# Kernel optimization log

Hardware: AMD Instinct MI355X
Metric: run time of the kernel (lower is better)

The kernel has to match this reference:

```python
import jax, jax.numpy as jnp
import numpy as np

K_DIM = 1024
HEADS = 16


def setup_inputs() -> dict:
    key = jax.random.key(0)
    ks = jax.random.split(key, 8)
    b, t, tc, k = 2, 2048, 2048, K_DIM
    scale = 1.0 / np.sqrt(k)
    x = jax.random.normal(ks[0], (b, t, k), dtype=jnp.float32)
    context = jax.random.normal(ks[1], (b, tc, k), dtype=jnp.float32)
    Wq = jax.random.normal(ks[2], (k, k), dtype=jnp.float32) * scale
    Wk = jax.random.normal(ks[3], (k, k), dtype=jnp.float32) * scale
    Wv = jax.random.normal(ks[4], (k, k), dtype=jnp.float32) * scale
    Wo = jax.random.normal(ks[5], (k, k), dtype=jnp.float32) * scale
    bo = jax.random.normal(ks[6], (k,), dtype=jnp.float32) * 0.01
    return {"x": x, "context": context, "Wq": Wq, "Wk": Wk, "Wv": Wv, "Wo": Wo, "bo": bo}


def reference(x, context, Wq, Wk, Wv, Wo, bo):
    b, t, e = x.shape
    tc = context.shape[1]
    h = HEADS
    s = e // h
    # Linear(k,k,bias=False): y = x @ W.T
    q = (x @ Wq.T).reshape(b, t, h, s)
    k_ = (context @ Wk.T).reshape(b, tc, h, s)
    v = (context @ Wv.T).reshape(b, tc, h, s)
    # scale q and k each by e**-0.25 (net 1/sqrt(e), note: full embed dim, not head dim)
    inv4 = e ** (-0.25)
    q = q * inv4
    k_ = k_ * inv4
    # scores: [b, h, t, tc]
    dot = jnp.einsum('bthd,bchd->bhtc', q, k_)
    attn = jax.nn.softmax(dot, axis=-1)
    out = jnp.einsum('bhtc,bchd->bthd', attn, v).reshape(b, t, e)
    return out @ Wo.T + bo
```

## Files before the change

kernel.cpp:

```cpp
#include <hip/hip_runtime.h>
#include <stdint.h>

typedef unsigned short u16;
typedef unsigned int u32;
typedef __attribute__((ext_vector_type(4))) float f32x4;
typedef __attribute__((ext_vector_type(16))) float f32x16;
typedef __attribute__((ext_vector_type(8))) __bf16 bf16x8;
typedef __attribute__((ext_vector_type(8))) u16 u16x8;

constexpr int NB = 2, NT = 2048, NTC = 2048, NE = 1024, NH = 16, ND = 64;
constexpr int MTOK = NB * NT;
constexpr int KDIM = NE;
constexpr float QK_SCALE = (float)(0.17677669529663687 * 1.2011224087864498);
constexpr float FIXED_M = 24.0f;

__device__ __forceinline__ u16 f2bf(float f) {
  union { float f; uint32_t u; } v; v.f = f;
  uint32_t r = v.u + 0x7FFFu + ((v.u >> 16) & 1u);
  return (u16)(r >> 16);
}

__device__ __forceinline__ float fexp2(float x) {
#if __has_builtin(__builtin_amdgcn_exp2f)
  return __builtin_amdgcn_exp2f(x);
#else
  return exp2f(x);
#endif
}

__device__ __forceinline__ u32 cvtpk(float lo, float hi) {
  u32 r;
  asm("v_cvt_pk_bf16_f32 %0, %1, %2" : "=v"(r) : "v"(lo), "v"(hi));
  return r;
}

__device__ __forceinline__ void plswap(u32& a, u32& b) {
  asm("v_permlane32_swap_b32 %0, %1" : "+v"(a), "+v"(b));
}

__device__ __forceinline__ void gload16(const void* g, void* lds) {
  __builtin_amdgcn_global_load_lds(
      (const __attribute__((address_space(1))) unsigned int*)g,
      (__attribute__((address_space(3))) unsigned int*)lds, 16, 0, 0);
}

__device__ __forceinline__ f32x4 mfma16x16(bf16x8 a, bf16x8 b, f32x4 c) {
  return __builtin_amdgcn_mfma_f32_16x16x32_bf16(a, b, c, 0, 0, 0);
}
__device__ __forceinline__ f32x16 mfma32x32(bf16x8 a, bf16x8 b, f32x16 c) {
  return __builtin_amdgcn_mfma_f32_32x32x16_bf16(a, b, c, 0, 0, 0);
}

__device__ __forceinline__ int swz(int row, int part) {
  return row * 128 + ((part ^ (row & 7)) << 4);
}

__device__ __forceinline__ u16x8 cast8(const float4* p, float scale) {
  float4 a = p[0], b = p[1];
  u16x8 r;
  r[0] = f2bf(a.x * scale); r[1] = f2bf(a.y * scale);
  r[2] = f2bf(a.z * scale); r[3] = f2bf(a.w * scale);
  r[4] = f2bf(b.x * scale); r[5] = f2bf(b.y * scale);
  r[6] = f2bf(b.z * scale); r[7] = f2bf(b.w * scale);
  return r;
}

__global__ void cast_all(const float* __restrict__ x, const float* __restrict__ ctx,
                         const float* __restrict__ Wq, const float* __restrict__ Wk,
                         const float* __restrict__ Wv, const float* __restrict__ Wo,
                         u16* __restrict__ xb, u16* __restrict__ cb,
                         u16* __restrict__ wb) {
  int i = blockIdx.x * blockDim.x + threadIdx.x;
  const float* src; u16* dst; int j; float scale = 1.0f;
  if (i < 524288) { src = x; dst = xb; j = i; }
  else if (i < 1048576) { src = ctx; dst = cb; j = i - 524288; }
  else {
    int k = i - 1048576;
    int which = k >> 17; j = k & 131071;
    src = (which == 0) ? Wq : (which == 1) ? Wk : (which == 2) ? Wv : Wo;
    scale = (which < 2) ? QK_SCALE : 1.0f;
    dst = wb + (size_t)which * (NE * KDIM);
  }
  *((u16x8*)dst + j) = cast8((const float4*)src + (size_t)j * 2, scale);
}

__global__ __launch_bounds__(256)
void gemm_qkv(const u16* __restrict__ xb, const u16* __restrict__ cb,
              const u16* __restrict__ wqb, const u16* __restrict__ wkvb,
              u16* __restrict__ Qb, u16* __restrict__ KVb) {
  __shared__ __align__(16) u16 Al[64 * 64];
  __shared__ __align__(16) u16 Bl[128 * 64];
  const int tid = threadIdx.x, w = tid >> 6, l = tid & 63;
  const int l15 = l & 15, l4 = l >> 4;
  const int wm = w >> 1, wn = w & 1;

  const int bid = blockIdx.x;
  const bool isQ = bid < 512;
  const u16* A; const u16* Bm; int mbase, nbase;
  if (isQ) { A = xb; Bm = wqb; nbase = (bid & 7) * 128; mbase = (bid >> 3) * 64; }
  else { int b2 = bid - 512; A = cb; Bm = wkvb; nbase = (b2 & 15) * 128; mbase = (b2 >> 4) * 64; }

  f32x4 acc[2][4] = {};
  const char* Ab = (const char*)(A + (size_t)mbase * KDIM);
  const char* Bb = (const char*)(Bm + (size_t)nbase * KDIM);

  for (int k0 = 0; k0 < KDIM; k0 += 64) {
#pragma unroll
    for (int s = 0; s < 2; ++s) {
      int i = (w * 2 + s) * 64 + l;
      int row = i >> 3, part = i & 7;
      int gofs = row * (KDIM * 2) + k0 * 2 + ((part ^ (row & 7)) << 4);
      gload16(Ab + gofs, (char*)Al + (w * 2 + s) * 1024);
    }
#pragma unroll
    for (int s = 0; s < 4; ++s) {
      int i = (w * 4 + s) * 64 + l;
      int row = i >> 3, part = i & 7;
      int gofs = row * (KDIM * 2) + k0 * 2 + ((part ^ (row & 7)) << 4);
      gload16(Bb + gofs, (char*)Bl + (w * 4 + s) * 1024);
    }
    __syncthreads();
#pragma unroll
    for (int kc = 0; kc < 2; ++kc) {
      bf16x8 af[2], bfr[4];
#pragma unroll
      for (int mt = 0; mt < 2; ++mt) {
        int r = wm * 32 + mt * 16 + l15;
        af[mt] = *(const bf16x8*)((const char*)Al + swz(r, kc * 4 + l4));
      }
#pragma unroll
      for (int nt = 0; nt < 4; ++nt) {
        int r = wn * 64 + nt * 16 + l15;
        bfr[nt] = *(const bf16x8*)((const char*)Bl + swz(r, kc * 4 + l4));
      }
#pragma unroll
      for (int mt = 0; mt < 2; ++mt)
#pragma unroll
        for (int nt = 0; nt < 4; ++nt)
          acc[mt][nt] = mfma16x16(af[mt], bfr[nt], acc[mt][nt]);
    }
    __syncthreads();
  }

#pragma unroll
  for (int mt = 0; mt < 2; ++mt) {
#pragma unroll
    for (int nt = 0; nt < 4; ++nt) {
      int col = nbase + wn * 64 + nt * 16 + l15;
      int mrow0 = mbase + wm * 32 + mt * 16 + l4 * 4;
#pragma unroll
      for (int r = 0; r < 4; ++r) {
        int m = mrow0 + r;
        float v = acc[mt][nt][r];
        if (isQ) {
          int b = m >> 11, t = m & (NT - 1), h = col >> 6, d = col & (ND - 1);
          Qb[((size_t)(b * NH + h) * NT + t) * ND + d] = f2bf(v);
        } else {
          int b = m >> 11, tc = m & (NTC - 1);
          int h = (col >> 6) & 15, d = col & (ND - 1);
          size_t base = ((size_t)((b * NH + h) * 32 + (tc >> 6))) * 4096;
          if (col < 1024) {
            size_t idx = base + (size_t)(d >> 3) * 512 + (size_t)(tc & 63) * 8 + (d & 7);
            KVb[idx] = f2bf(v);
          } else {
            size_t idx = base + (size_t)((tc & 63) >> 3) * 512 + (size_t)d * 8 + (tc & 7);
            KVb[4194304 + idx] = f2bf(v);
          }
        }
      }
    }
  }
}

__device__ __forceinline__ void gemm_loop(const char* Ab, const char* Bb,
                                          u16* Al, u16* Bl, int tid,
                                          f32x4 (&acc)[2][4]) {
  const int w = tid >> 6, l = tid & 63;
  const int l15 = l & 15, l4 = l >> 4;
  const int wm = w >> 1, wn = w & 1;

  auto stage = [&](int buf, int k0) {
#pragma unroll
    for (int s = 0; s < 2; ++s) {
      int i = (w * 2 + s) * 64 + l;
      int row = i >> 3, part = i & 7;
      int gofs = row * (KDIM * 2) + k0 * 2 + ((part ^ (row & 7)) << 4);
      gload16(Ab + gofs, (char*)(Al + buf * 4096) + (w * 2 + s) * 1024);
    }
#pragma unroll
    for (int s = 0; s < 4; ++s) {
      int i = (w * 4 + s) * 64 + l;
      int row = i >> 3, part = i & 7;
      int gofs = row * (KDIM * 2) + k0 * 2 + ((part ^ (row & 7)) << 4);
      gload16(Bb + gofs, (char*)(Bl + buf * 8192) + (w * 4 + s) * 1024);
    }
  };

  stage(0, 0);
  stage(1, 64);

  for (int it = 0; it < 16; ++it) {
    const int cur = it & 1;
    if (it < 15) asm volatile("s_waitcnt vmcnt(6)" ::: "memory");
    else         asm volatile("s_waitcnt vmcnt(0)" ::: "memory");
    __builtin_amdgcn_s_barrier();
    const char* Ac = (const char*)(Al + cur * 4096);
    const char* Bc = (const char*)(Bl + cur * 8192);
#pragma unroll
    for (int kc = 0; kc < 2; ++kc) {
      bf16x8 af[2], bfr[4];
#pragma unroll
      for (int mt = 0; mt < 2; ++mt)
        af[mt] = *(const bf16x8*)(Ac + swz(wm * 32 + mt * 16 + l15, kc * 4 + l4));
#pragma unroll
      for (int nt = 0; nt < 4; ++nt)
        bfr[nt] = *(const bf16x8*)(Bc + swz(wn * 64 + nt * 16 + l15, kc * 4 + l4));
#pragma unroll
      for (int mt = 0; mt < 2; ++mt)
#pragma unroll
        for (int nt = 0; nt < 4; ++nt)
          acc[mt][nt] = mfma16x16(af[mt], bfr[nt], acc[mt][nt]);
    }
    __builtin_amdgcn_s_barrier();
    if (it < 14) stage(cur, (it + 2) * 64);
  }
}

__global__ __launch_bounds__(256)
void gemm_out(const u16* __restrict__ A, const u16* __restrict__ Bm,
              float* __restrict__ Cout, const float* __restrict__ bias) {
  __shared__ __align__(16) u16 Al[2][64 * 64];
  __shared__ __align__(16) u16 Bl[2][128 * 64];
  const int tid = threadIdx.x, w = tid >> 6, l = tid & 63;
  const int l15 = l & 15, l4 = l >> 4;
  const int wm = w >> 1, wn = w & 1;

  int bid = blockIdx.x;
  bid = (bid & 7) * 64 + (bid >> 3);
  const int mbase = (bid >> 3) * 64, nbase = (bid & 7) * 128;

  f32x4 acc[2][4] = {};
  gemm_loop((const char*)(A + (size_t)mbase * KDIM),
            (const char*)(Bm + (size_t)nbase * KDIM),
            &Al[0][0], &Bl[0][0], tid, acc);

#pragma unroll
  for (int mt = 0; mt < 2; ++mt) {
#pragma unroll
    for (int nt = 0; nt < 4; ++nt) {
      int col = nbase + wn * 64 + nt * 16 + l15;
      int mrow0 = mbase + wm * 32 + mt * 16 + l4 * 4;
#pragma unroll
      for (int r = 0; r < 4; ++r)
        Cout[(size_t)(mrow0 + r) * NE + col] = acc[mt][nt][r] + bias[col];
    }
  }
}

__global__ __launch_bounds__(128, 2)
void attn_fwd(const u16* __restrict__ Q, const u16* __restrict__ K,
              const u16* __restrict__ Vt, u16* __restrict__ O) {
  __shared__ float Ol[64 * 64];
  __shared__ float Ll[64];
  const int tid = threadIdx.x, wid = tid >> 6, l = tid & 63;
  const int l31 = l & 31, hi = l >> 5;

  int n = blockIdx.x;
  int work = (n & 7) * 128 + (n >> 3);
  const int bh = work >> 5, qx = work & 31;
  const int b = bh >> 4, h = bh & 15;
  const int qbase = qx * 64;

  const char* Kb = (const char*)(K + (size_t)bh * 32 * 4096);
  const char* Vb = (const char*)(Vt + (size_t)bh * 32 * 4096);
  const u16* Qb = Q + (size_t)bh * NT * ND;

  auto kaddr = [&](int t32, int kc) {
    return Kb + (size_t)(t32 >> 1) * 8192 + (size_t)(kc * 2 + hi) * 1024
              + (size_t)((t32 & 1) * 32 + l31) * 16;
  };
  auto vaddr = [&](int t32, int j) {
    return Vb + (size_t)(t32 >> 1) * 8192
              + (size_t)((t32 & 1) * 4 + (j >> 1) * 2 + hi) * 1024
              + (size_t)((j & 1) * 32 + l31) * 16;
  };

  bf16x8 qf[2][4];
#pragma unroll
  for (int qt = 0; qt < 2; ++qt)
#pragma unroll
    for (int kc = 0; kc < 4; ++kc)
      qf[qt][kc] = *(const bf16x8*)(Qb + (size_t)(qbase + qt * 32 + l31) * ND + kc * 16 + hi * 8);

  f32x16 oacc[2][2] = {};
  f32x16 lacc[2] = {};
  f32x16 minit;
#pragma unroll
  for (int r = 0; r < 16; ++r) minit[r] = -FIXED_M;

  const int tbase = wid * 32;

  bf16x8 kfA[4], kfB[4], vf[4];
#pragma unroll
  for (int kc = 0; kc < 4; ++kc) kfA[kc] = *(const bf16x8*)kaddr(tbase, kc);

  for (int it2 = 0; it2 < 16; ++it2) {
    const int tA = tbase + it2 * 2, tB = tA + 1;

#pragma unroll
    for (int j = 0; j < 4; ++j) vf[j] = *(const bf16x8*)vaddr(tA, j);
#pragma unroll
    for (int kc = 0; kc < 4; ++kc) kfB[kc] = *(const bf16x8*)kaddr(tB, kc);
#pragma unroll
    for (int qt = 0; qt < 2; ++qt) {
      f32x16 sv = minit;
#pragma unroll
      for (int kc = 0; kc < 4; ++kc) sv = mfma32x32(kfA[kc], qf[qt][kc], sv);
#pragma unroll
      for (int r = 0; r < 16; ++r) { sv[r] = fexp2(sv[r]); lacc[qt][r] += sv[r]; }
      bf16x8 pa0, pa1;
      {
        u32 a1 = cvtpk(sv[0], sv[1]), b1 = cvtpk(sv[4], sv[5]);
        u32 a2 = cvtpk(sv[2], sv[3]), b2 = cvtpk(sv[6], sv[7]);
        plswap(a1, b1); plswap(a2, b2);
        u32 a3 = cvtpk(sv[8], sv[9]), b3 = cvtpk(sv[12], sv[13]);
        u32 a4 = cvtpk(sv[10], sv[11]), b4 = cvtpk(sv[14], sv[15]);
        plswap(a3, b3); plswap(a4, b4);
        union { u32 u[4]; bf16x8 v; } ua, ub;
        ua.u[0] = a1; ua.u[1] = a2; ua.u[2] = b1; ua.u[3] = b2;
        ub.u[0] = a3; ub.u[1] = a4; ub.u[2] = b3; ub.u[3] = b4;
        pa0 = ua.v; pa1 = ub.v;
      }
      oacc[qt][0] = mfma32x32(pa0, vf[0], oacc[qt][0]);
      oacc[qt][1] = mfma32x32(pa0, vf[1], oacc[qt][1]);
      oacc[qt][0] = mfma32x32(pa1, vf[2], oacc[qt][0]);
      oacc[qt][1] = mfma32x32(pa1, vf[3], oacc[qt][1]);
    }

#pragma unroll
    for (int j = 0; j < 4; ++j) vf[j] = *(const bf16x8*)vaddr(tB, j);
#pragma unroll
    for (int kc = 0; kc < 4; ++kc) kfA[kc] = *(const bf16x8*)kaddr(tB + 1, kc);
#pragma unroll
    for (int qt = 0; qt < 2; ++qt) {
      f32x16 sv = minit;
#pragma unroll
      for (int kc = 0; kc < 4; ++kc) sv = mfma32x32(kfB[kc], qf[qt][kc], sv);
#pragma unroll
      for (int r = 0; r < 16; ++r) { sv[r] = fexp2(sv[r]); lacc[qt][r] += sv[r]; }
      bf16x8 pa0, pa1;
      {
        u32 a1 = cvtpk(sv[0], sv[1]), b1 = cvtpk(sv[4], sv[5]);
        u32 a2 = cvtpk(sv[2], sv[3]), b2 = cvtpk(sv[6], sv[7]);
        plswap(a1, b1); plswap(a2, b2);
        u32 a3 = cvtpk(sv[8], sv[9]), b3 = cvtpk(sv[12], sv[13]);
        u32 a4 = cvtpk(sv[10], sv[11]), b4 = cvtpk(sv[14], sv[15]);
        plswap(a3, b3); plswap(a4, b4);
        union { u32 u[4]; bf16x8 v; } ua, ub;
        ua.u[0] = a1; ua.u[1] = a2; ua.u[2] = b1; ua.u[3] = b2;
        ub.u[0] = a3; ub.u[1] = a4; ub.u[2] = b3; ub.u[3] = b4;
        pa0 = ua.v; pa1 = ub.v;
      }
      oacc[qt][0] = mfma32x32(pa0, vf[0], oacc[qt][0]);
      oacc[qt][1] = mfma32x32(pa0, vf[1], oacc[qt][1]);
      oacc[qt][0] = mfma32x32(pa1, vf[2], oacc[qt][0]);
      oacc[qt][1] = mfma32x32(pa1, vf[3], oacc[qt][1]);
    }
  }

  float lsum[2];
#pragma unroll
  for (int qt = 0; qt < 2; ++qt) {
    f32x16 t = lacc[qt];
#pragma unroll
    for (int s = 8; s >= 1; s >>= 1)
#pragma unroll
      for (int r = 0; r < s; ++r) t[r] += t[r + s];
    lsum[qt] = t[0] + __shfl_xor(t[0], 32);
  }

  if (wid == 1) {
#pragma unroll
    for (int qt = 0; qt < 2; ++qt) {
#pragma unroll
      for (int r = 0; r < 16; ++r) {
        int crow = (r & 3) + 8 * (r >> 2) + 4 * hi;
        Ol[(qt * 32 + crow) * 64 + l31] = oacc[qt][0][r];
        Ol[(qt * 32 + crow) * 64 + 32 + l31] = oacc[qt][1][r];
      }
      if (!hi) Ll[qt * 32 + l31] = lsum[qt];
    }
  }
  __syncthreads();
  if (wid == 0) {
#pragma unroll
    for (int qt = 0; qt < 2; ++qt) {
      float inv = 1.0f / (lsum[qt] + Ll[qt * 32 + l31]);
#pragma unroll
      for (int r = 0; r < 16; ++r) {
        int crow = (r & 3) + 8 * (r >> 2) + 4 * hi;
        float ir = __shfl(inv, crow);
        int t = qbase + qt * 32 + crow;
        size_t rowo = (size_t)(b * NT + t) * NE + h * 64 + l31;
        O[rowo] = f2bf((oacc[qt][0][r] + Ol[(qt * 32 + crow) * 64 + l31]) * ir);
        O[rowo + 32] = f2bf((oacc[qt][1][r] + Ol[(qt * 32 + crow) * 64 + 32 + l31]) * ir);
      }
    }
  }
}

extern "C" void kernel_launch(void* const* d_in, const int* in_sizes, int n_in,
                              void* d_out, int out_size, void* d_ws, size_t ws_size,
                              hipStream_t stream) {
  const float* x   = (const float*)d_in[0];
  const float* ctx = (const float*)d_in[1];
  const float* Wq  = (const float*)d_in[2];
  const float* Wk  = (const float*)d_in[3];
  const float* Wv  = (const float*)d_in[4];
  const float* Wo  = (const float*)d_in[5];
  const float* bo  = (const float*)d_in[6];
  float* out = (float*)d_out;
  char* ws = (char*)d_ws;

  u16* xb  = (u16*)(ws);
  u16* cb  = (u16*)(ws + (8u  << 20));
  u16* wqb = (u16*)(ws + (16u << 20));
  u16* wkb = (u16*)(ws + (18u << 20));
  u16* wob = (u16*)(ws + (22u << 20));
  u16* Qb  = (u16*)(ws + (24u << 20));
  u16* Kb  = (u16*)(ws + (32u << 20));
  u16* Vtb = (u16*)(ws + (40u << 20));
  u16* Ob  = (u16*)(ws + (48u << 20));

  cast_all<<<6144, 256, 0, stream>>>(x, ctx, Wq, Wk, Wv, Wo, xb, cb, wqb);
  gemm_qkv<<<1536, 256, 0, stream>>>(xb, cb, wqb, wkb, Qb, Kb);
  attn_fwd<<<1024, 128, 0, stream>>>(Qb, Kb, Vtb, Ob);
  gemm_out<<<512, 256, 0, stream>>>(Ob, wob, out, bo);
}
```

Before: 112.6 us.

## Split attention KV range across two blocks with atomic merge

Splits each attention work item's context range into two halves handled by separate blocks. Partial unnormalized outputs and row sums go into fp32 buffers via atomicAdd, and a new merge kernel normalizes them and writes bf16. This doubles the grid to 2048 blocks for better CU occupancy and load balance. The cost is a memset, atomic traffic, an extra kernel launch and fp32 round-trip memory, with the workspace reused over the xb/cb region after it is consumed.

Result: slower. 146.8 us (+30.4%).

```diff
diff --git a/kernel.cpp b/kernel.cpp
--- a/kernel.cpp
+++ b/kernel.cpp
@@ -258,17 +258,18 @@
 }
 
 __global__ __launch_bounds__(128, 2)
-void attn_fwd(const u16* __restrict__ Q, const u16* __restrict__ K,
-              const u16* __restrict__ Vt, u16* __restrict__ O) {
+void attn_part(const u16* __restrict__ Q, const u16* __restrict__ K,
+               const u16* __restrict__ Vt, float* __restrict__ Oacc,
+               float* __restrict__ Lacc) {
   __shared__ float Ol[64 * 64];
   __shared__ float Ll[64];
   const int tid = threadIdx.x, wid = tid >> 6, l = tid & 63;
   const int l31 = l & 31, hi = l >> 5;
 
   int n = blockIdx.x;
-  int work = (n & 7) * 128 + (n >> 3);
-  const int bh = work >> 5, qx = work & 31;
-  const int b = bh >> 4, h = bh & 15;
+  int work = (n & 7) * 256 + (n >> 3);
+  const int bh = work >> 6, rem = work & 63;
+  const int qx = rem >> 1, half = rem & 1;
   const int qbase = qx * 64;
 
   const char* Kb = (const char*)(K + (size_t)bh * 32 * 4096);
@@ -298,13 +299,13 @@
 #pragma unroll
   for (int r = 0; r < 16; ++r) minit[r] = -FIXED_M;
 
-  const int tbase = wid * 32;
+  const int tbase = half * 32 + wid * 16;
 
   bf16x8 kfA[4], kfB[4], vf[4];
 #pragma unroll
   for (int kc = 0; kc < 4; ++kc) kfA[kc] = *(const bf16x8*)kaddr(tbase, kc);
 
-  for (int it2 = 0; it2 < 16; ++it2) {
+  for (int it2 = 0; it2 < 8; ++it2) {
     const int tA = tbase + it2 * 2, tB = tA + 1;
 
 #pragma unroll
@@ -395,18 +396,34 @@
   if (wid == 0) {
 #pragma unroll
     for (int qt = 0; qt < 2; ++qt) {
-      float inv = 1.0f / (lsum[qt] + Ll[qt * 32 + l31]);
+      float ls = lsum[qt] + Ll[qt * 32 + l31];
+      if (!hi) atomicAdd(&Lacc[bh * NT + qbase + qt * 32 + l31], ls);
 #pragma unroll
       for (int r = 0; r < 16; ++r) {
         int crow = (r & 3) + 8 * (r >> 2) + 4 * hi;
-        float ir = __shfl(inv, crow);
         int t = qbase + qt * 32 + crow;
-        size_t rowo = (size_t)(b * NT + t) * NE + h * 64 + l31;
-        O[rowo] = f2bf((oacc[qt][0][r] + Ol[(qt * 32 + crow) * 64 + l31]) * ir);
-        O[rowo + 32] = f2bf((oacc[qt][1][r] + Ol[(qt * 32 + crow) * 64 + 32 + l31]) * ir);
-      }
-    }
-  }
+        float v0 = oacc[qt][0][r] + Ol[(qt * 32 + crow) * 64 + l31];
+        float v1 = oacc[qt][1][r] + Ol[(qt * 32 + crow) * 64 + 32 + l31];
+        atomicAdd(&Oacc[((size_t)bh * NT + t) * 64 + l31], v0);
+        atomicAdd(&Oacc[((size_t)bh * NT + t) * 64 + 32 + l31], v1);
+      }
+    }
+  }
+}
+
+__global__ void attn_merge(const float* __restrict__ Oacc, const float* __restrict__ Lacc,
+                           u16* __restrict__ O) {
+  int i = blockIdx.x * blockDim.x + threadIdx.x;
+  int d8 = i & 7;
+  int t = (i >> 3) & (NT - 1);
+  int bh = i >> 14;
+  int b = bh >> 4, h = bh & 15;
+  const float* src = Oacc + ((size_t)bh * NT + t) * 64 + d8 * 8;
+  float inv = 1.0f / Lacc[bh * NT + t];
+  u16x8 r;
+#pragma unroll
+  for (int j = 0; j < 8; ++j) r[j] = f2bf(src[j] * inv);
+  *(u16x8*)(O + ((size_t)(b * NT + t)) * NE + h * 64 + d8 * 8) = r;
 }
 
 extern "C" void kernel_launch(void* const* d_in, const int* in_sizes, int n_in,
@@ -431,9 +448,13 @@
   u16* Kb  = (u16*)(ws + (32u << 20));
   u16* Vtb = (u16*)(ws + (40u << 20));
   u16* Ob  = (u16*)(ws + (48u << 20));
+  float* Oacc = (float*)(ws);
+  float* Lacc = (float*)(ws + (16u << 20));
 
   cast_all<<<6144, 256, 0, stream>>>(x, ctx, Wq, Wk, Wv, Wo, xb, cb, wqb);
   gemm_qkv<<<1536, 256, 0, stream>>>(xb, cb, wqb, wkb, Qb, Kb);
-  attn_fwd<<<1024, 128, 0, stream>>>(Qb, Kb, Vtb, Ob);
+  hipMemsetAsync(ws, 0, (16u << 20) + (256u << 10), stream);
+  attn_part<<<2048, 128, 0, stream>>>(Qb, Kb, Vtb, Oacc, Lacc);
+  attn_merge<<<2048, 256, 0, stream>>>(Oacc, Lacc, Ob);
   gemm_out<<<512, 256, 0, stream>>>(Ob, wob, out, bo);
 }
```
